# Kernel optimization log

Measured on AMD Instinct MI355X. Metric: run time of the kernel, lower is better.

## Reference

```python
import jax, jax.numpy as jnp
import numpy as np

B = 16384
H = 1024

def setup_inputs() -> dict:
    key = jax.random.key(0)
    k1, k2, k3, k4, k5 = jax.random.split(key, 5)
    inp = jax.random.normal(k1, (B, 3 * H), dtype=jnp.float32)
    previous_state = jax.random.normal(k2, (B, H), dtype=jnp.float32)
    mask = jax.random.uniform(k3, (B,), dtype=jnp.float32)
    # params: th_normal scale 0.08
    Wur = 0.08 * jax.random.normal(k4, (H, 2 * H), dtype=jnp.float32)
    U = 0.08 * jax.random.normal(k5, (H, H), dtype=jnp.float32)
    return {"inp": inp, "previous_state": previous_state, "mask": mask, "Wur": Wur, "U": U}

def reference(inp, previous_state, mask, Wur, U):
    h = U.shape[0]
    state_inp = inp[:, :h]            # [B, H]
    gate_inp = inp[:, h:]             # [B, 2H]
    gates = jax.nn.sigmoid(previous_state @ Wur + gate_inp)  # [B, 2H]
    update = gates[:, :h]
    reset = gates[:, h:]
    p = (state_inp * reset) @ U       # [B, H]
    next_state = jnp.tanh(p + state_inp)
    # NOTE: faithful to source (additive combine, not convex blend)
    next_state_f = next_state + update + (previous_state + (1.0 - update))
    m = mask[:, None]
    return m * next_state_f + (1.0 - m) * previous_state
```

## Files before the change

kernel.cpp:

```cpp
#include <hip/hip_runtime.h>
#include <cstdint>
#include <cstddef>

#define DI __device__ __forceinline__

typedef __attribute__((ext_vector_type(8))) short short8;
typedef __attribute__((ext_vector_type(4))) float floatx4;

static constexpr int BATCH = 16384;
static constexpr int H = 1024;
static constexpr int NT = H / 64;
static constexpr int HALF = 128 * 64;

DI unsigned short f32_to_bf16_bits(float x) {
  union { float f; unsigned int u; } c; c.f = x;
  unsigned int r = c.u + 0x7fffu + ((c.u >> 16) & 1u);
  return (unsigned short)(r >> 16);
}

__global__ __launch_bounds__(256) void cast_bf16_kernel(const float* __restrict__ in,
                                                        unsigned short* __restrict__ out) {
  const int i = (blockIdx.x * 256 + threadIdx.x) * 8;
  const float4 v0 = *reinterpret_cast<const float4*>(in + i);
  const float4 v1 = *reinterpret_cast<const float4*>(in + i + 4);
  short8 o;
  o[0] = (short)f32_to_bf16_bits(v0.x);
  o[1] = (short)f32_to_bf16_bits(v0.y);
  o[2] = (short)f32_to_bf16_bits(v0.z);
  o[3] = (short)f32_to_bf16_bits(v0.w);
  o[4] = (short)f32_to_bf16_bits(v1.x);
  o[5] = (short)f32_to_bf16_bits(v1.y);
  o[6] = (short)f32_to_bf16_bits(v1.z);
  o[7] = (short)f32_to_bf16_bits(v1.w);
  *reinterpret_cast<short8*>(out + i) = o;
}

__global__ __launch_bounds__(256) void transpose_cast2_kernel(const float* __restrict__ Wur,
                                                              const float* __restrict__ U,
                                                              unsigned short* __restrict__ WrT,
                                                              unsigned short* __restrict__ UT) {
  __shared__ float tile[32][33];
  const float* in;
  unsigned short* out;
  int src_stride, src_col0;
  if (blockIdx.z == 0) {
    in = Wur; out = WrT; src_stride = 2 * H; src_col0 = H;
  } else {
    in = U; out = UT; src_stride = H; src_col0 = 0;
  }
  const int bx = blockIdx.x * 32;
  const int by = blockIdx.y * 32;
  const int tx = threadIdx.x;
  const int ty = threadIdx.y;
#pragma unroll
  for (int i = 0; i < 32; i += 8)
    tile[ty + i][tx] = in[(size_t)(bx + ty + i) * src_stride + src_col0 + by + tx];
  __syncthreads();
#pragma unroll
  for (int i = 0; i < 32; i += 8)
    out[(size_t)(by + ty + i) * H + bx + tx] = f32_to_bf16_bits(tile[tx][ty + i]);
}

DI void ld8(short8* fr, const unsigned short* base, int wofs, int l16, int q) {
  const int x7 = l16 & 7;
#pragma unroll
  for (int f = 0; f < 4; ++f) {
    const int lr = 32 * f + wofs + l16;
#pragma unroll
    for (int ks = 0; ks < 2; ++ks)
      fr[f * 2 + ks] = *(const short8*)&base[lr * 64 + (((ks * 4 + q) ^ x7) * 8)];
  }
}
DI void ld4(short8* fr, const unsigned short* base, int wofs, int l16, int q) {
  const int x7 = l16 & 7;
#pragma unroll
  for (int jj = 0; jj < 2; ++jj) {
    const int lc = 64 * jj + wofs + l16;
#pragma unroll
    for (int ks = 0; ks < 2; ++ks)
      fr[jj * 2 + ks] = *(const short8*)&base[lc * 64 + (((ks * 4 + q) ^ x7) * 8)];
  }
}

template <int IO, int JO>
DI void mma16(floatx4 (&acc)[8][4], const short8* af, const short8* bf) {
#pragma unroll
  for (int ks = 0; ks < 2; ++ks)
#pragma unroll
    for (int f = 0; f < 4; ++f)
#pragma unroll
      for (int jj = 0; jj < 2; ++jj)
        acc[IO + f][JO + jj] = __builtin_amdgcn_mfma_f32_16x16x32_bf16(
            af[f * 2 + ks], bf[jj * 2 + ks], acc[IO + f][JO + jj], 0, 0, 0);
}

template <int EPI>
__global__ __launch_bounds__(512, 2) void gemm_fused(const unsigned short* __restrict__ A,
                                                     const unsigned short* __restrict__ Bt,
                                                     const float* __restrict__ inp,
                                                     const float* __restrict__ prev,
                                                     const float* __restrict__ mask,
                                                     unsigned short* __restrict__ Xout,
                                                     float* __restrict__ Out) {
  __shared__ __align__(16) unsigned short ldsA[2 * 2 * HALF];
  __shared__ __align__(16) unsigned short ldsB[2 * 2 * HALF];

  const int tid = threadIdx.x;
  const int lane = tid & 63;
  const int w = tid >> 6;
  const int wm16 = (w >> 2) * 16;
  const int wn16 = (w & 3) * 16;
  const int q = lane >> 4;
  const int l16 = lane & 15;

  const int sid = blockIdx.y * gridDim.x + blockIdx.x;
  const int lid = (sid & 7) * 32 + (sid >> 3);
  const int blockN = (lid & 3) * 256;
  const int blockM = (lid >> 2) * 256;

  int srcoff[2], dstch[2];
#pragma unroll
  for (int n = 0; n < 2; ++n) {
    const int c = n * 512 + tid;
    const int r = c >> 3;
    const int gc = (c & 7) ^ (r & 7);
    srcoff[n] = r * H + gc * 8;
    dstch[n] = n * 512 + w * 64;
  }

  const unsigned short* Ab = A + (size_t)blockM * H;
  const unsigned short* Bb = Bt + (size_t)blockN * H;

  auto stage = [&](const unsigned short* gsrc, unsigned short* ldst) {
#pragma unroll
    for (int n = 0; n < 2; ++n) {
      __builtin_amdgcn_global_load_lds(
          (const __attribute__((address_space(1))) unsigned int*)(gsrc + srcoff[n]),
          (__attribute__((address_space(3))) unsigned int*)(ldst + dstch[n] * 8), 16, 0, 0);
    }
  };

  floatx4 acc[8][4] = {};
  short8 af[8], bf0[4], bf1[4];

  stage(Ab, ldsA);
  stage(Bb, ldsB);
  stage(Bb + 128 * H, ldsB + HALF);
  stage(Ab + 128 * H, ldsA + HALF);
  asm volatile("s_waitcnt vmcnt(4)" ::: "memory");
  __builtin_amdgcn_s_barrier();

  for (int t = 0; t < NT; ++t) {
    const int cur = t & 1;
    const int kn = ((t + 1) & (NT - 1)) * 64;
    const unsigned short* lAc = ldsA + cur * 2 * HALF;
    const unsigned short* lBc = ldsB + cur * 2 * HALF;
    unsigned short* lAn = ldsA + (cur ^ 1) * 2 * HALF;
    unsigned short* lBn = ldsB + (cur ^ 1) * 2 * HALF;

    ld8(af, lAc, wm16, l16, q);
    ld4(bf0, lBc, wn16, l16, q);
    stage(Ab + kn, lAn);
    __builtin_amdgcn_s_barrier();
    __builtin_amdgcn_s_setprio(1);
    mma16<0, 0>(acc, af, bf0);
    __builtin_amdgcn_s_setprio(0);
    asm volatile("s_waitcnt vmcnt(4)" ::: "memory");
    __builtin_amdgcn_s_barrier();

    ld4(bf1, lBc + HALF, wn16, l16, q);
    stage(Bb + kn, lBn);
    __builtin_amdgcn_s_barrier();
    __builtin_amdgcn_s_setprio(1);
    mma16<0, 2>(acc, af, bf1);
    __builtin_amdgcn_s_setprio(0);
    asm volatile("s_waitcnt vmcnt(4)" ::: "memory");
    __builtin_amdgcn_s_barrier();

    ld8(af, lAc + HALF, wm16, l16, q);
    stage(Bb + 128 * H + kn, lBn + HALF);
    __builtin_amdgcn_s_barrier();
    __builtin_amdgcn_s_setprio(1);
    mma16<4, 2>(acc, af, bf1);
    __builtin_amdgcn_s_setprio(0);
    __builtin_amdgcn_s_barrier();

    stage(Ab + 128 * H + kn, lAn + HALF);
    __builtin_amdgcn_s_barrier();
    __builtin_amdgcn_s_setprio(1);
    mma16<4, 0>(acc, af, bf0);
    __builtin_amdgcn_s_setprio(0);
    asm volatile("s_waitcnt vmcnt(4)" ::: "memory");
    __builtin_amdgcn_s_barrier();
  }

#pragma unroll
  for (int i = 0; i < 8; ++i) {
    const int gr0 = blockM + 128 * (i >> 2) + 32 * (i & 3) + wm16 + q * 4;
#pragma unroll
    for (int j = 0; j < 4; ++j) {
      const int gcol = blockN + 128 * (j >> 1) + 64 * (j & 1) + wn16 + l16;
#pragma unroll
      for (int rg = 0; rg < 4; ++rg) {
        const int gr = gr0 + rg;
        const float v = acc[i][j][rg];
        if (EPI == 0) {
          const float z = v + inp[(size_t)gr * (3 * H) + 2 * H + gcol];
          const float rst = 1.0f / (1.0f + __expf(-z));
          const float x = inp[(size_t)gr * (3 * H) + gcol] * rst;
          Xout[(size_t)gr * H + gcol] = f32_to_bf16_bits(x);
        } else {
          const float s = inp[(size_t)gr * (3 * H) + gcol];
          const float a = v + s;
          const float ns = 1.0f - 2.0f / (__expf(2.0f * a) + 1.0f);
          const float m = mask[gr];
          Out[(size_t)gr * H + gcol] = m * (ns + 1.0f) + prev[(size_t)gr * H + gcol];
        }
      }
    }
  }
}

extern "C" void kernel_launch(void* const* d_in, const int* in_sizes, int n_in,
                              void* d_out, int out_size, void* d_ws, size_t ws_size,
                              hipStream_t stream) {
  const float* inp = (const float*)d_in[0];
  const float* prev = (const float*)d_in[1];
  const float* mask = (const float*)d_in[2];
  const float* Wur = (const float*)d_in[3];
  const float* U = (const float*)d_in[4];
  float* out = (float*)d_out;

  char* ws = (char*)d_ws;
  unsigned short* prevb = (unsigned short*)ws;
  unsigned short* Xb = (unsigned short*)(ws + (size_t)BATCH * H * 2);
  unsigned short* WrT = (unsigned short*)(ws + (size_t)BATCH * H * 4);
  unsigned short* UT = WrT + (size_t)H * H;

  cast_bf16_kernel<<<(BATCH * H) / (256 * 8), 256, 0, stream>>>(prev, prevb);
  transpose_cast2_kernel<<<dim3(H / 32, H / 32, 2), dim3(32, 8), 0, stream>>>(Wur, U, WrT, UT);

  gemm_fused<0><<<dim3(H / 256, BATCH / 256), 512, 0, stream>>>(prevb, WrT, inp, nullptr,
                                                                nullptr, Xb, nullptr);
  gemm_fused<1><<<dim3(H / 256, BATCH / 256), 512, 0, stream>>>(Xb, UT, inp, prev, mask,
                                                                nullptr, out);
}
```

Baseline: 422.3 us.

## Fuse fp32-to-bf16 cast of previous_state into first GEMM's A-tile loading

Drops the standalone cast kernel that turned previous_state into bf16 in workspace. A new 128x128-tile GEMM kernel now loads fp32 previous_state directly into registers, converts it to bf16 and writes it into swizzled LDS. B tiles are brought in with global_load_lds, and the sigmoid/reset epilogue is kept. This removes one full read/write pass over a 16384x1024 activation and one launch. In exchange the first GEMM uses a simpler, smaller-tile pipeline than the tuned 256x256 kernel and does the conversion inside its main loop.

```diff
diff --git a/kernel.cpp b/kernel.cpp
--- a/kernel.cpp
+++ b/kernel.cpp
@@ -16,23 +16,6 @@
   union { float f; unsigned int u; } c; c.f = x;
   unsigned int r = c.u + 0x7fffu + ((c.u >> 16) & 1u);
   return (unsigned short)(r >> 16);
-}
-
-__global__ __launch_bounds__(256) void cast_bf16_kernel(const float* __restrict__ in,
-                                                        unsigned short* __restrict__ out) {
-  const int i = (blockIdx.x * 256 + threadIdx.x) * 8;
-  const float4 v0 = *reinterpret_cast<const float4*>(in + i);
-  const float4 v1 = *reinterpret_cast<const float4*>(in + i + 4);
-  short8 o;
-  o[0] = (short)f32_to_bf16_bits(v0.x);
-  o[1] = (short)f32_to_bf16_bits(v0.y);
-  o[2] = (short)f32_to_bf16_bits(v0.z);
-  o[3] = (short)f32_to_bf16_bits(v0.w);
-  o[4] = (short)f32_to_bf16_bits(v1.x);
-  o[5] = (short)f32_to_bf16_bits(v1.y);
-  o[6] = (short)f32_to_bf16_bits(v1.z);
-  o[7] = (short)f32_to_bf16_bits(v1.w);
-  *reinterpret_cast<short8*>(out + i) = o;
 }
 
 __global__ __launch_bounds__(256) void transpose_cast2_kernel(const float* __restrict__ Wur,
@@ -61,6 +44,130 @@
     out[(size_t)(by + ty + i) * H + bx + tx] = f32_to_bf16_bits(tile[tx][ty + i]);
 }
 
+__global__ __launch_bounds__(256, 2) void gemm_k1(const float* __restrict__ prevf,
+                                                  const unsigned short* __restrict__ Bt,
+                                                  const float* __restrict__ inp,
+                                                  unsigned short* __restrict__ Xout) {
+  __shared__ __align__(16) unsigned short ldsA[2][128 * 64];
+  __shared__ __align__(16) unsigned short ldsB[2][128 * 64];
+
+  const int tid = threadIdx.x;
+  const int lane = tid & 63;
+  const int wave = tid >> 6;
+  const int wm = wave >> 1;
+  const int wn = wave & 1;
+  const int q = lane >> 4;
+  const int l16 = lane & 15;
+
+  const int sid = blockIdx.y * gridDim.x + blockIdx.x;
+  const int lid = (sid & 7) * 128 + (sid >> 3);
+  const int bx = lid & 7;
+  const int by = lid >> 3;
+  const int blockM = by * 128;
+  const int blockN = bx * 128;
+
+  int aRow[4], aKlog[4], bSrc[4], bDst[4];
+#pragma unroll
+  for (int j = 0; j < 4; ++j) {
+    const int c = j * 256 + tid;
+    const int r = c >> 3;
+    aRow[j] = r;
+    aKlog[j] = ((c & 7) ^ (r & 7)) * 8;
+    bSrc[j] = r * H + aKlog[j];
+    bDst[j] = (j * 256 + (wave << 6)) * 8;
+  }
+
+  auto issueA = [&](int kt, float4* st) {
+#pragma unroll
+    for (int j = 0; j < 4; ++j) {
+      const float* s = prevf + (size_t)(blockM + aRow[j]) * H + kt + aKlog[j];
+      st[2 * j] = *reinterpret_cast<const float4*>(s);
+      st[2 * j + 1] = *reinterpret_cast<const float4*>(s + 4);
+    }
+  };
+  auto issueB = [&](int kt, int buf) {
+#pragma unroll
+    for (int j = 0; j < 4; ++j) {
+      __builtin_amdgcn_global_load_lds(
+          (const __attribute__((address_space(1))) unsigned int*)(Bt + (size_t)blockN * H + kt + bSrc[j]),
+          (__attribute__((address_space(3))) unsigned int*)(&ldsB[buf][bDst[j]]), 16, 0, 0);
+    }
+  };
+  auto writeA = [&](const float4* st, int buf) {
+#pragma unroll
+    for (int j = 0; j < 4; ++j) {
+      const int c = j * 256 + tid;
+      short8 o;
+      o[0] = (short)f32_to_bf16_bits(st[2 * j].x);
+      o[1] = (short)f32_to_bf16_bits(st[2 * j].y);
+      o[2] = (short)f32_to_bf16_bits(st[2 * j].z);
+      o[3] = (short)f32_to_bf16_bits(st[2 * j].w);
+      o[4] = (short)f32_to_bf16_bits(st[2 * j + 1].x);
+      o[5] = (short)f32_to_bf16_bits(st[2 * j + 1].y);
+      o[6] = (short)f32_to_bf16_bits(st[2 * j + 1].z);
+      o[7] = (short)f32_to_bf16_bits(st[2 * j + 1].w);
+      *reinterpret_cast<short8*>(&ldsA[buf][c * 8]) = o;
+    }
+  };
+
+  floatx4 acc[4][4] = {};
+  float4 st[8];
+
+  issueA(0, st);
+  issueB(0, 0);
+  writeA(st, 0);
+  __syncthreads();
+
+  for (int t = 0; t < NT; ++t) {
+    const int cur = t & 1;
+    const int kn = ((t + 1) & (NT - 1)) * 64;
+    issueA(kn, st);
+    issueB(kn, cur ^ 1);
+
+#pragma unroll
+    for (int ks = 0; ks < 2; ++ks) {
+      short8 af[4], bfr[4];
+#pragma unroll
+      for (int i = 0; i < 4; ++i) {
+        const int r = wm * 64 + i * 16 + l16;
+        const int ch = ks * 4 + q;
+        af[i] = *(const short8*)&ldsA[cur][(r * 8 + (ch ^ (r & 7))) * 8];
+      }
+#pragma unroll
+      for (int j = 0; j < 4; ++j) {
+        const int r = wn * 64 + j * 16 + l16;
+        const int ch = ks * 4 + q;
+        bfr[j] = *(const short8*)&ldsB[cur][(r * 8 + (ch ^ (r & 7))) * 8];
+      }
+#pragma unroll
+      for (int i = 0; i < 4; ++i)
+#pragma unroll
+        for (int j = 0; j < 4; ++j)
+          acc[i][j] = __builtin_amdgcn_mfma_f32_16x16x32_bf16(af[i], bfr[j], acc[i][j], 0, 0, 0);
+    }
+
+    writeA(st, cur ^ 1);
+    __syncthreads();
+  }
+
+#pragma unroll
+  for (int i = 0; i < 4; ++i) {
+    const int gr0 = blockM + wm * 64 + i * 16 + q * 4;
+#pragma unroll
+    for (int j = 0; j < 4; ++j) {
+      const int gcol = blockN + wn * 64 + j * 16 + l16;
+#pragma unroll
+      for (int rg = 0; rg < 4; ++rg) {
+        const int gr = gr0 + rg;
+        const float z = acc[i][j][rg] + inp[(size_t)gr * (3 * H) + 2 * H + gcol];
+        const float rst = 1.0f / (1.0f + __expf(-z));
+        const float x = inp[(size_t)gr * (3 * H) + gcol] * rst;
+        Xout[(size_t)gr * H + gcol] = f32_to_bf16_bits(x);
+      }
+    }
+  }
+}
+
 DI void ld8(short8* fr, const unsigned short* base, int wofs, int l16, int q) {
   const int x7 = l16 & 7;
 #pragma unroll
@@ -94,14 +201,12 @@
             af[f * 2 + ks], bf[jj * 2 + ks], acc[IO + f][JO + jj], 0, 0, 0);
 }
 
-template <int EPI>
-__global__ __launch_bounds__(512, 2) void gemm_fused(const unsigned short* __restrict__ A,
-                                                     const unsigned short* __restrict__ Bt,
-                                                     const float* __restrict__ inp,
-                                                     const float* __restrict__ prev,
-                                                     const float* __restrict__ mask,
-                                                     unsigned short* __restrict__ Xout,
-                                                     float* __restrict__ Out) {
+__global__ __launch_bounds__(512, 2) void gemm_k2(const unsigned short* __restrict__ A,
+                                                  const unsigned short* __restrict__ Bt,
+                                                  const float* __restrict__ inp,
+                                                  const float* __restrict__ prev,
+                                                  const float* __restrict__ mask,
+                                                  float* __restrict__ Out) {
   __shared__ __align__(16) unsigned short ldsA[2 * 2 * HALF];
   __shared__ __align__(16) unsigned short ldsB[2 * 2 * HALF];
 
@@ -203,19 +308,11 @@
 #pragma unroll
       for (int rg = 0; rg < 4; ++rg) {
         const int gr = gr0 + rg;
-        const float v = acc[i][j][rg];
-        if (EPI == 0) {
-          const float z = v + inp[(size_t)gr * (3 * H) + 2 * H + gcol];
-          const float rst = 1.0f / (1.0f + __expf(-z));
-          const float x = inp[(size_t)gr * (3 * H) + gcol] * rst;
-          Xout[(size_t)gr * H + gcol] = f32_to_bf16_bits(x);
-        } else {
-          const float s = inp[(size_t)gr * (3 * H) + gcol];
-          const float a = v + s;
-          const float ns = 1.0f - 2.0f / (__expf(2.0f * a) + 1.0f);
-          const float m = mask[gr];
-          Out[(size_t)gr * H + gcol] = m * (ns + 1.0f) + prev[(size_t)gr * H + gcol];
-        }
+        const float s = inp[(size_t)gr * (3 * H) + gcol];
+        const float a = acc[i][j][rg] + s;
+        const float ns = 1.0f - 2.0f / (__expf(2.0f * a) + 1.0f);
+        const float m = mask[gr];
+        Out[(size_t)gr * H + gcol] = m * (ns + 1.0f) + prev[(size_t)gr * H + gcol];
       }
     }
   }
@@ -232,16 +329,13 @@
   float* out = (float*)d_out;
 
   char* ws = (char*)d_ws;
-  unsigned short* prevb = (unsigned short*)ws;
-  unsigned short* Xb = (unsigned short*)(ws + (size_t)BATCH * H * 2);
-  unsigned short* WrT = (unsigned short*)(ws + (size_t)BATCH * H * 4);
+  unsigned short* Xb = (unsigned short*)ws;
+  unsigned short* WrT = (unsigned short*)(ws + (size_t)BATCH * H * 2);
   unsigned short* UT = WrT + (size_t)H * H;
 
-  cast_bf16_kernel<<<(BATCH * H) / (256 * 8), 256, 0, stream>>>(prev, prevb);
   transpose_cast2_kernel<<<dim3(H / 32, H / 32, 2), dim3(32, 8), 0, stream>>>(Wur, U, WrT, UT);
 
-  gemm_fused<0><<<dim3(H / 256, BATCH / 256), 512, 0, stream>>>(prevb, WrT, inp, nullptr,
-                                                                nullptr, Xb, nullptr);
-  gemm_fused<1><<<dim3(H / 256, BATCH / 256), 512, 0, stream>>>(Xb, UT, inp, prev, mask,
-                                                                nullptr, out);
-}
+  gemm_k1<<<dim3(H / 128, BATCH / 128), 256, 0, stream>>>(prev, WrT, inp, Xb);
+
+  gemm_k2<<<dim3(H / 256, BATCH / 256), 512, 0, stream>>>(Xb, UT, inp, prev, mask, out);
+}
```

After: 459.1 us. 8.7% more time.
